# Optimization experiments

Hardware: AMD Instinct MI355X
Metric: run time of the kernel (lower is better)

## Reference

```python
import jax, jax.numpy as jnp
import numpy as np

B, SQ, SK, D, H = 2, 2048, 2048, 1024, 16
DK = D // H


def setup_inputs() -> dict:
    key = jax.random.key(0)
    ks = jax.random.split(key, 9)
    query = jax.random.normal(ks[0], (B, SQ, D), dtype=jnp.float32)
    k_in = jax.random.normal(ks[1], (B, SK, D), dtype=jnp.float32)
    v_in = jax.random.normal(ks[2], (B, SK, D), dtype=jnp.float32)
    # padding mask: 1 for valid tokens, 0 for padding; lengths in [SK//2, SK]
    lengths = jax.random.randint(ks[3], (B,), SK // 2, SK + 1)
    mask = (jnp.arange(SK)[None, :] < lengths[:, None]).astype(jnp.int32)
    scale = 1.0 / np.sqrt(D)
    Wq = jax.random.normal(ks[4], (D, D), dtype=jnp.float32) * scale
    Wk = jax.random.normal(ks[5], (D, D), dtype=jnp.float32) * scale
    Wv = jax.random.normal(ks[6], (D, D), dtype=jnp.float32) * scale
    Wo = jax.random.normal(ks[7], (D, D), dtype=jnp.float32) * scale
    return {"query": query, "key": k_in, "value": v_in, "mask": mask,
            "Wq": Wq, "Wk": Wk, "Wv": Wv, "Wo": Wo}


def reference(query, key, value, mask, Wq, Wk, Wv, Wo):
    # linear projections (torch Linear: x @ W.T)
    q = (query @ Wq.T).reshape(B, SQ, H, DK).transpose(0, 2, 1, 3)  # [B,H,SQ,DK]
    k = (key @ Wk.T).reshape(B, SK, H, DK).transpose(0, 2, 1, 3)    # [B,H,SK,DK]
    v = (value @ Wv.T).reshape(B, SK, H, DK).transpose(0, 2, 1, 3)  # [B,H,SK,DK]
    scores = jnp.einsum('bhqd,bhkd->bhqk', q, k) / jnp.sqrt(jnp.float32(DK))
    # padding mask: (B, SK) -> (B, 1, 1, SK)
    scores = jnp.where(mask[:, None, None, :] == 0, -jnp.inf, scores)
    # future (causal) mask
    future = jnp.triu(jnp.ones((SQ, SK), dtype=bool), k=1)
    scores = jnp.where(future[None, None], -jnp.inf, scores)
    attn = jax.nn.softmax(scores, axis=-1)
    attn = jnp.nan_to_num(attn, nan=0.0)
    ctx = jnp.einsum('bhqk,bhkd->bhqd', attn, v)
    ctx = ctx.transpose(0, 2, 1, 3).reshape(B, SQ, D)
    return ctx @ Wo.T
```

## Files before the change

### kernel.cpp

```cpp
#include <hip/hip_runtime.h>
#include <hip/hip_bf16.h>
#include <stdint.h>

#define BB 2
#define SS 2048
#define DD 1024
#define HH 16
#define DKK 64
#define MM (BB*SS)
#define LOG2E 1.4426950408889634f
#define QSCALE (0.125f * LOG2E)

typedef __attribute__((ext_vector_type(8))) short short8;
typedef __attribute__((ext_vector_type(8))) _Float16 half8;
typedef __attribute__((ext_vector_type(4))) float f32x4;

__device__ __forceinline__ short bfr(float f) {
    return (short)((__float_as_uint(f) + 0x8000u) >> 16);
}
__device__ __forceinline__ short f2h(float f) {
    _Float16 h = (_Float16)f;
    return __builtin_bit_cast(short, h);
}
__device__ __forceinline__ short8 cvt8(float4 a, float4 b) {
    short8 s;
    s[0] = bfr(a.x); s[1] = bfr(a.y); s[2] = bfr(a.z); s[3] = bfr(a.w);
    s[4] = bfr(b.x); s[5] = bfr(b.y); s[6] = bfr(b.z); s[7] = bfr(b.w);
    return s;
}

__device__ __forceinline__ void dma16(const void* g, void* l) {
    __builtin_amdgcn_global_load_lds(
        (const __attribute__((address_space(1))) uint32_t*)g,
        (__attribute__((address_space(3))) uint32_t*)(uintptr_t)l, 16, 0, 0);
}


__global__ __launch_bounds__(256) void cvt_all(const float* __restrict__ q,
                                               const float* __restrict__ k,
                                               const float* __restrict__ v,
                                               const float* __restrict__ wq,
                                               const float* __restrict__ wk,
                                               const float* __restrict__ wv,
                                               const float* __restrict__ wo,
                                               const int* __restrict__ mask,
                                               short* __restrict__ dst,
                                               float* __restrict__ Fb) {
    const size_t nth = (size_t)gridDim.x * blockDim.x;
    const size_t tid = (size_t)blockIdx.x * blockDim.x + threadIdx.x;
    if (tid < BB * SS) Fb[tid] = mask[tid] ? 0.f : -30000.f;
    for (size_t i8 = tid; i8 < (1u << 21); i8 += nth) {
        const size_t e = i8 * 8;
        const float* s;
        size_t rel;
        if (e < 4194304)        { s = q; rel = e; }
        else if (e < 8388608)   { s = k; rel = e - 4194304; }
        else if (e < 12582912)  { s = v; rel = e - 8388608; }
        else {
            const size_t we = e - 12582912;
            s = (we < 1048576) ? wq : (we < 2097152) ? wk : (we < 3145728) ? wv : wo;
            rel = we & 1048575;
        }
        const float4* p = (const float4*)(s + rel);
        *(short8*)(dst + e) = cvt8(p[0], p[1]);
    }
}

__global__ __launch_bounds__(256) void qkv_lds(const short* __restrict__ Abf,
                                               const short* __restrict__ Wbf,
                                               short* __restrict__ Qb,
                                               short* __restrict__ Kb,
                                               short* __restrict__ Vtb) {
    __shared__ __align__(16) short SH[128 * 132];
    short* As = SH;
    short* Ws = SH + 8192;
    const int z = blockIdx.z;
    const short* A = Abf + (size_t)z * 4194304;
    const short* W = Wbf + (size_t)z * 1048576;
    const int t = threadIdx.x, wave = t >> 6, lane = t & 63;
    const int la = lane & 15, quad = lane >> 4;
    const int wm = wave & 1, wn = wave >> 1;
    const int m0 = blockIdx.x * 128, n0 = blockIdx.y * 128;

    f32x4 acc[4][4];
    #pragma unroll
    for (int i = 0; i < 4; ++i)
        #pragma unroll
        for (int j = 0; j < 4; ++j) acc[i][j] = {0.f, 0.f, 0.f, 0.f};

    for (int k0 = 0; k0 < DD; k0 += 64) {
        #pragma unroll
        for (int j = 0; j < 4; ++j) {
            const int idx = j * 256 + t;
            const int row = idx >> 3, cpos = idx & 7;
            const int gc = cpos ^ (row & 7);
            dma16(A + (size_t)(m0 + row) * DD + k0 + gc * 8, As + idx * 8);
            dma16(W + (size_t)(n0 + row) * DD + k0 + gc * 8, Ws + idx * 8);
        }
        __syncthreads();
        #pragma unroll
        for (int kh = 0; kh < 2; ++kh) {
            short8 af[4], bf[4];
            #pragma unroll
            for (int mt = 0; mt < 4; ++mt) {
                const int row = wm * 64 + mt * 16 + la;
                af[mt] = *(const short8*)&As[row * 64 + (((kh << 2) | quad) ^ (row & 7)) * 8];
            }
            #pragma unroll
            for (int nt = 0; nt < 4; ++nt) {
                const int row = wn * 64 + nt * 16 + la;
                bf[nt] = *(const short8*)&Ws[row * 64 + (((kh << 2) | quad) ^ (row & 7)) * 8];
            }
            #pragma unroll
            for (int mt = 0; mt < 4; ++mt)
                #pragma unroll
                for (int nt = 0; nt < 4; ++nt)
                    acc[mt][nt] = __builtin_amdgcn_mfma_f32_16x16x32_bf16(af[mt], bf[nt], acc[mt][nt], 0, 0, 0);
        }
        __syncthreads();
    }

    #pragma unroll
    for (int mt = 0; mt < 4; ++mt)
        #pragma unroll
        for (int nt = 0; nt < 4; ++nt)
            #pragma unroll
            for (int r = 0; r < 4; ++r) {
                const float v = acc[mt][nt][r];
                const int mr = wm * 64 + mt * 16 + quad * 4 + r;
                const int nc = wn * 64 + nt * 16 + la;
                if (z == 2) SH[nc * 132 + mr] = f2h(v);
                else        SH[mr * 132 + nc] = bfr(z == 0 ? v * QSCALE : v);
            }
    __syncthreads();

    const int b = m0 >> 11;
    #pragma unroll
    for (int p = 0; p < 8; ++p) {
        const int idx = p * 256 + t;
        const int rr = idx >> 4, c8 = (idx & 15) * 8;
        short8 val = *(const short8*)&SH[rr * 132 + c8];
        if (z == 2) {
            const int n = n0 + rr, h2 = n >> 6, dk = n & 63;
            const int s = (m0 & 2047) + c8;
            *(short8*)(Vtb + ((size_t)(b * HH + h2) * DKK + dk) * SS + s) = val;
        } else {
            const int s = (m0 + rr) & 2047;
            const int n = n0 + c8, h2 = n >> 6, dk = n & 63;
            short* Y = (z == 0) ? Qb : Kb;
            *(short8*)(Y + ((size_t)(b * HH + h2) * SS + s) * DKK + dk) = val;
        }
    }
}

__global__ __launch_bounds__(256, 4) void attn4(const short* __restrict__ Q,
                                                const short* __restrict__ K,
                                                const short* __restrict__ Vt,
                                                const float* __restrict__ Fb,
                                                short* __restrict__ ctx) {
    const int b = blockIdx.z, h = blockIdx.y;
    const int qt = 15 - blockIdx.x;
    const int t = threadIdx.x, wave = t >> 6, lane = t & 63;
    const int la = lane & 15, quad = lane >> 4;

    __shared__ __align__(16) short Ks[64 * 72];
    __shared__ __align__(16) short Vs[64 * 72];
    __shared__ __align__(16) short Ps[128 * 76];

    const size_t kbase = ((size_t)(b * HH + h) * SS) * DKK;
    const size_t vbase = ((size_t)(b * HH + h) * DKK) * SS;

    short8 aq[2][2];
    #pragma unroll
    for (int mt = 0; mt < 2; ++mt)
        #pragma unroll
        for (int hf = 0; hf < 2; ++hf)
            aq[mt][hf] = *(const short8*)(Q + kbase
                + (size_t)(qt * 128 + wave * 32 + mt * 16 + la) * DKK + hf * 32 + quad * 8);

    const int srow = t >> 2, scol = (t & 3) * 16;
    short8 kr[2], vr[2];
    auto loadG = [&](int kt) {
        const short* kp = K + kbase + (size_t)(kt * 64 + srow) * DKK + scol;
        kr[0] = ((const short8*)kp)[0]; kr[1] = ((const short8*)kp)[1];
        const short* vp = Vt + vbase + (size_t)srow * SS + kt * 64 + scol;
        vr[0] = ((const short8*)vp)[0]; vr[1] = ((const short8*)vp)[1];
    };
    auto storeL = [&]() {
        *(short8*)&Ks[srow * 72 + scol]     = kr[0];
        *(short8*)&Ks[srow * 72 + scol + 8] = kr[1];
        *(short8*)&Vs[srow * 72 + scol]     = vr[0];
        *(short8*)&Vs[srow * 72 + scol + 8] = vr[1];
    };

    float rs[2][4] = {};
    f32x4 o[2][4];
    #pragma unroll
    for (int mt = 0; mt < 2; ++mt)
        #pragma unroll
        for (int dc = 0; dc < 4; ++dc) o[mt][dc] = {0.f, 0.f, 0.f, 0.f};

    const int lastkt = 2 * qt + 1;
    loadG(0); storeL(); __syncthreads();

    for (int kt = 0; kt <= lastkt; ++kt) {
        if (kt < lastkt) loadG(kt + 1);
        const bool diag   = (kt >= 2 * qt);
        const bool padded = (kt >= 16);

        #pragma unroll
        for (int ct = 0; ct < 4; ++ct) {
            short8 kb0 = *(const short8*)&Ks[(ct * 16 + la) * 72 + quad * 8];
            short8 kb1 = *(const short8*)&Ks[(ct * 16 + la) * 72 + 32 + quad * 8];
            f32x4 s[2];
            #pragma unroll
            for (int mt = 0; mt < 2; ++mt) {
                s[mt] = {0.f, 0.f, 0.f, 0.f};
                s[mt] = __builtin_amdgcn_mfma_f32_16x16x32_bf16(aq[mt][0], kb0, s[mt], 0, 0, 0);
                s[mt] = __builtin_amdgcn_mfma_f32_16x16x32_bf16(aq[mt][1], kb1, s[mt], 0, 0, 0);
            }
            const int col = kt * 64 + ct * 16 + la;
            const float bias = padded ? Fb[b * SS + col] : 0.f;
            #pragma unroll
            for (int mt = 0; mt < 2; ++mt) {
                const int row0 = qt * 128 + wave * 32 + mt * 16 + quad * 4;
                #pragma unroll
                for (int r = 0; r < 4; ++r) {
                    float x = s[mt][r] + bias;
                    if (diag && col > row0 + r) x = -30000.f;
                    const float p = exp2f(x);
                    rs[mt][r] += p;
                    Ps[(wave * 32 + mt * 16 + quad * 4 + r) * 76 + ct * 16 + la] = f2h(p);
                }
            }
        }

        #pragma unroll
        for (int c2 = 0; c2 < 2; ++c2) {
            half8 pa0 = *(const half8*)&Ps[(wave * 32 + la) * 76 + c2 * 32 + quad * 8];
            half8 pa1 = *(const half8*)&Ps[(wave * 32 + 16 + la) * 76 + c2 * 32 + quad * 8];
            #pragma unroll
            for (int dc = 0; dc < 4; ++dc) {
                half8 vb = *(const half8*)&Vs[(dc * 16 + la) * 72 + c2 * 32 + quad * 8];
                o[0][dc] = __builtin_amdgcn_mfma_f32_16x16x32_f16(pa0, vb, o[0][dc], 0, 0, 0);
                o[1][dc] = __builtin_amdgcn_mfma_f32_16x16x32_f16(pa1, vb, o[1][dc], 0, 0, 0);
            }
        }

        if (kt < lastkt) {
            __syncthreads();
            storeL();
            __syncthreads();
        }
    }

    #pragma unroll
    for (int mt = 0; mt < 2; ++mt) {
        #pragma unroll
        for (int r = 0; r < 4; ++r) {
            float v = rs[mt][r];
            v += __shfl_xor(v, 1, 64);
            v += __shfl_xor(v, 2, 64);
            v += __shfl_xor(v, 4, 64);
            v += __shfl_xor(v, 8, 64);
            const float inv = 1.0f / v;
            const int q = qt * 128 + wave * 32 + mt * 16 + quad * 4 + r;
            #pragma unroll
            for (int dc = 0; dc < 4; ++dc)
                ctx[((size_t)(b * SS + q) * DD) + h * DKK + dc * 16 + la] = bfr(o[mt][dc][r] * inv);
        }
    }
}

__global__ __launch_bounds__(256) void o_lds(const short* __restrict__ Ctx,
                                             const short* __restrict__ Wob,
                                             float* __restrict__ out) {
    __shared__ __align__(16) short As[128 * 64];
    __shared__ __align__(16) short Ws[64 * 64];
    const int t = threadIdx.x, wave = t >> 6, lane = t & 63;
    const int la = lane & 15, quad = lane >> 4;
    const int wm = wave & 1, wn = wave >> 1;
    const int m0 = blockIdx.x * 128, n0 = blockIdx.y * 64;

    f32x4 acc[4][2];
    #pragma unroll
    for (int i = 0; i < 4; ++i)
        #pragma unroll
        for (int j = 0; j < 2; ++j) acc[i][j] = {0.f, 0.f, 0.f, 0.f};

    for (int k0 = 0; k0 < DD; k0 += 64) {
        #pragma unroll
        for (int j = 0; j < 4; ++j) {
            const int idx = j * 256 + t;
            const int row = idx >> 3, cpos = idx & 7;
            const int gc = cpos ^ (row & 7);
            dma16(Ctx + (size_t)(m0 + row) * DD + k0 + gc * 8, (short*)As + idx * 8);
        }
        #pragma unroll
        for (int j = 0; j < 2; ++j) {
            const int idx = j * 256 + t;
            const int row = idx >> 3, cpos = idx & 7;
            const int gc = cpos ^ (row & 7);
            dma16(Wob + (size_t)(n0 + row) * DD + k0 + gc * 8, (short*)Ws + idx * 8);
        }
        __syncthreads();
        #pragma unroll
        for (int kh = 0; kh < 2; ++kh) {
            short8 af[4], bf[2];
            #pragma unroll
            for (int mt = 0; mt < 4; ++mt) {
                const int row = wm * 64 + mt * 16 + la;
                af[mt] = *(const short8*)&As[row * 64 + (((kh << 2) | quad) ^ (row & 7)) * 8];
            }
            #pragma unroll
            for (int nt = 0; nt < 2; ++nt) {
                const int row = wn * 32 + nt * 16 + la;
                bf[nt] = *(const short8*)&Ws[row * 64 + (((kh << 2) | quad) ^ (row & 7)) * 8];
            }
            #pragma unroll
            for (int mt = 0; mt < 4; ++mt)
                #pragma unroll
                for (int nt = 0; nt < 2; ++nt)
                    acc[mt][nt] = __builtin_amdgcn_mfma_f32_16x16x32_bf16(af[mt], bf[nt], acc[mt][nt], 0, 0, 0);
        }
        __syncthreads();
    }

    #pragma unroll
    for (int mt = 0; mt < 4; ++mt)
        #pragma unroll
        for (int nt = 0; nt < 2; ++nt)
            #pragma unroll
            for (int r = 0; r < 4; ++r) {
                const int m = m0 + wm * 64 + mt * 16 + quad * 4 + r;
                const int n = n0 + wn * 32 + nt * 16 + la;
                out[(size_t)m * DD + n] = acc[mt][nt][r];
            }
}

__global__ __launch_bounds__(256) void qkv_gemm(const float* __restrict__ Aq,
                                                const float* __restrict__ Ak,
                                                const float* __restrict__ Av,
                                                const float* __restrict__ Wq,
                                                const float* __restrict__ Wk,
                                                const float* __restrict__ Wv,
                                                short* __restrict__ Qb,
                                                short* __restrict__ Kb,
                                                short* __restrict__ Vtb) {
    __shared__ __align__(16) short As[2][128][40];
    __shared__ __align__(16) short Ws[2][128][40];
    const int z = blockIdx.z;
    const float* A = (z == 0) ? Aq : (z == 1) ? Ak : Av;
    const float* W = (z == 0) ? Wq : (z == 1) ? Wk : Wv;
    short* Y = (z == 0) ? Qb : (z == 1) ? Kb : Vtb;
    const int t = threadIdx.x, wave = t >> 6, lane = t & 63;
    const int la = lane & 15, quad = lane >> 4;
    const int wm = wave & 1, wn = wave >> 1;
    const int m0 = blockIdx.x * 128, n0 = blockIdx.y * 128;
    const int srow = t >> 1, scol = (t & 1) * 16;
    f32x4 acc[4][4];
    #pragma unroll
    for (int i = 0; i < 4; ++i)
        #pragma unroll
        for (int j = 0; j < 4; ++j) acc[i][j] = {0.f, 0.f, 0.f, 0.f};
    float4 ar[4], wr[4];
    auto loadG = [&](int i) {
        const int k0 = i * 32;
        const float4* pa = (const float4*)(A + (size_t)(m0 + srow) * DD + k0 + scol);
        ar[0] = pa[0]; ar[1] = pa[1]; ar[2] = pa[2]; ar[3] = pa[3];
        const float4* pw = (const float4*)(W + (size_t)(n0 + srow) * DD + k0 + scol);
        wr[0] = pw[0]; wr[1] = pw[1]; wr[2] = pw[2]; wr[3] = pw[3];
    };
    auto storeL = [&](int buf) {
        *(short8*)&As[buf][srow][scol]     = cvt8(ar[0], ar[1]);
        *(short8*)&As[buf][srow][scol + 8] = cvt8(ar[2], ar[3]);
        *(short8*)&Ws[buf][srow][scol]     = cvt8(wr[0], wr[1]);
        *(short8*)&Ws[buf][srow][scol + 8] = cvt8(wr[2], wr[3]);
    };
    loadG(0); storeL(0); __syncthreads();
    const int NIT = DD / 32;
    for (int i = 0; i < NIT; ++i) {
        if (i + 1 < NIT) loadG(i + 1);
        const int buf = i & 1;
        short8 af[4], bfv[4];
        #pragma unroll
        for (int mt = 0; mt < 4; ++mt)
            af[mt] = *(const short8*)&As[buf][wm * 64 + mt * 16 + la][quad * 8];
        #pragma unroll
        for (int nt = 0; nt < 4; ++nt)
            bfv[nt] = *(const short8*)&Ws[buf][wn * 64 + nt * 16 + la][quad * 8];
        #pragma unroll
        for (int mt = 0; mt < 4; ++mt)
            #pragma unroll
            for (int nt = 0; nt < 4; ++nt)
                acc[mt][nt] = __builtin_amdgcn_mfma_f32_16x16x32_bf16(af[mt], bfv[nt], acc[mt][nt], 0, 0, 0);
        if (i + 1 < NIT) { storeL((i + 1) & 1); __syncthreads(); }
    }
    #pragma unroll
    for (int mt = 0; mt < 4; ++mt)
        #pragma unroll
        for (int nt = 0; nt < 4; ++nt)
            #pragma unroll
            for (int r = 0; r < 4; ++r) {
                const int m = m0 + wm * 64 + mt * 16 + quad * 4 + r;
                const int n = n0 + wn * 64 + nt * 16 + la;
                const int b = m >> 11, s = m & (SS - 1);
                const int h = n >> 6, dk = n & 63;
                float v = acc[mt][nt][r];
                if (z == 0)      Y[(((size_t)(b * HH + h) * SS + s) * DKK) + dk] = bfr(v * QSCALE);
                else if (z == 1) Y[(((size_t)(b * HH + h) * SS + s) * DKK) + dk] = bfr(v);
                else             Y[(((size_t)(b * HH + h) * DKK + dk) * SS) + s] = bfr(v);
            }
}

__global__ __launch_bounds__(256) void attn_fused(const short* __restrict__ Q,
                                                  const short* __restrict__ K,
                                                  const short* __restrict__ Vt,
                                                  const int* __restrict__ mask,
                                                  short* __restrict__ ctx) {
    const int b = blockIdx.z, h = blockIdx.y, x = blockIdx.x;
    const int t = threadIdx.x, wave = t >> 6, lane = t & 63;
    const int la = lane & 15, quad = lane >> 4;
    __shared__ __align__(16) short Ks[2][64][72];
    __shared__ __align__(16) short Vs[2][64][72];
    __shared__ __align__(16) short Ps[64][72];
    const size_t kbase = ((size_t)(b * HH + h) * SS) * DKK;
    const size_t vbase = ((size_t)(b * HH + h) * DKK) * SS;
    const int srow = t >> 2, scol = (t & 3) * 16;
    short8 kr[2], vr[2];
    auto loadG = [&](int kt) {
        const short* kp = K + kbase + (size_t)(kt * 64 + srow) * DKK + scol;
        kr[0] = ((const short8*)kp)[0]; kr[1] = ((const short8*)kp)[1];
        const short* vp = Vt + vbase + (size_t)srow * SS + kt * 64 + scol;
        vr[0] = ((const short8*)vp)[0]; vr[1] = ((const short8*)vp)[1];
    };
    auto storeL = [&](int buf) {
        *(short8*)&Ks[buf][srow][scol]     = kr[0];
        *(short8*)&Ks[buf][srow][scol + 8] = kr[1];
        *(short8*)&Vs[buf][srow][scol]     = vr[0];
        *(short8*)&Vs[buf][srow][scol + 8] = vr[1];
    };
    #pragma unroll 1
    for (int phase = 0; phase < 2; ++phase) {
        const int qt = phase ? x : (31 - x);
        const size_t qbase = kbase + (size_t)(qt * 64) * DKK;
        const short8 aq0 = *(const short8*)(Q + qbase + (size_t)(wave * 16 + la) * DKK + quad * 8);
        const short8 aq1 = *(const short8*)(Q + qbase + (size_t)(wave * 16 + la) * DKK + 32 + quad * 8);
        float rs[4] = {0.f, 0.f, 0.f, 0.f};
        f32x4 o[4];
        #pragma unroll
        for (int dc = 0; dc < 4; ++dc) o[dc] = {0.f, 0.f, 0.f, 0.f};
        const int nkt = qt + 1;
        loadG(0); storeL(0); __syncthreads();
        for (int kt = 0; kt < nkt; ++kt) {
            if (kt + 1 < nkt) loadG(kt + 1);
            const int buf = kt & 1;
            const bool diag = (kt == qt);
            const bool padded = (kt >= 16);
            f32x4 s[4];
            #pragma unroll
            for (int ct = 0; ct < 4; ++ct) {
                s[ct] = {0.f, 0.f, 0.f, 0.f};
                short8 kb0 = *(const short8*)&Ks[buf][ct * 16 + la][quad * 8];
                short8 kb1 = *(const short8*)&Ks[buf][ct * 16 + la][32 + quad * 8];
                s[ct] = __builtin_amdgcn_mfma_f32_16x16x32_bf16(aq0, kb0, s[ct], 0, 0, 0);
                s[ct] = __builtin_amdgcn_mfma_f32_16x16x32_bf16(aq1, kb1, s[ct], 0, 0, 0);
            }
            const int rowq = qt * 64 + wave * 16 + quad * 4;
            #pragma unroll
            for (int ct = 0; ct < 4; ++ct) {
                const int col = kt * 64 + ct * 16 + la;
                const int mv = padded ? mask[b * SS + col] : 1;
                #pragma unroll
                for (int r = 0; r < 4; ++r) {
                    const bool dead = (diag && col > rowq + r) || (padded && mv == 0);
                    const float p = dead ? 0.f : exp2f(s[ct][r]);
                    rs[r] += p;
                    Ps[wave * 16 + quad * 4 + r][ct * 16 + la] = bfr(p);
                }
            }
            #pragma unroll
            for (int c2 = 0; c2 < 2; ++c2) {
                short8 pa = *(const short8*)&Ps[wave * 16 + la][c2 * 32 + quad * 8];
                #pragma unroll
                for (int dc = 0; dc < 4; ++dc) {
                    short8 vb = *(const short8*)&Vs[buf][dc * 16 + la][c2 * 32 + quad * 8];
                    o[dc] = __builtin_amdgcn_mfma_f32_16x16x32_bf16(pa, vb, o[dc], 0, 0, 0);
                }
            }
            if (kt + 1 < nkt) { storeL((kt + 1) & 1); __syncthreads(); }
        }
        #pragma unroll
        for (int r = 0; r < 4; ++r) {
            float v = rs[r];
            v += __shfl_xor(v, 1, 64);
            v += __shfl_xor(v, 2, 64);
            v += __shfl_xor(v, 4, 64);
            v += __shfl_xor(v, 8, 64);
            const float inv = 1.0f / v;
            const int q = qt * 64 + wave * 16 + quad * 4 + r;
            #pragma unroll
            for (int dc = 0; dc < 4; ++dc)
                ctx[((size_t)(b * SS + q) * DD) + h * DKK + dc * 16 + la] = bfr(o[dc][r] * inv);
        }
        __syncthreads();
    }
}

__global__ __launch_bounds__(256) void o_gemm(const short* __restrict__ Ctx,
                                              const float* __restrict__ Wo,
                                              float* __restrict__ out) {
    __shared__ __align__(16) short As[2][128][40];
    __shared__ __align__(16) short Ws[2][64][40];
    const int t = threadIdx.x, wave = t >> 6, lane = t & 63;
    const int la = lane & 15, quad = lane >> 4;
    const int wm = wave & 1, wn = wave >> 1;
    const int m0 = blockIdx.x * 128, n0 = blockIdx.y * 64;
    const int srowA = t >> 1, scolA = (t & 1) * 16;
    const int srowW = t >> 2, scolW = (t & 3) * 8;
    f32x4 acc[4][2];
    #pragma unroll
    for (int i = 0; i < 4; ++i)
        #pragma unroll
        for (int j = 0; j < 2; ++j) acc[i][j] = {0.f, 0.f, 0.f, 0.f};
    short8 ab[2];
    float4 wr[2];
    auto loadG = [&](int i) {
        const int k0 = i * 32;
        const short8* pa = (const short8*)(Ctx + (size_t)(m0 + srowA) * DD + k0 + scolA);
        ab[0] = pa[0]; ab[1] = pa[1];
        const float4* pw = (const float4*)(Wo + (size_t)(n0 + srowW) * DD + k0 + scolW);
        wr[0] = pw[0]; wr[1] = pw[1];
    };
    auto storeL = [&](int buf) {
        *(short8*)&As[buf][srowA][scolA]     = ab[0];
        *(short8*)&As[buf][srowA][scolA + 8] = ab[1];
        *(short8*)&Ws[buf][srowW][scolW]     = cvt8(wr[0], wr[1]);
    };
    loadG(0); storeL(0); __syncthreads();
    const int NIT = DD / 32;
    for (int i = 0; i < NIT; ++i) {
        if (i + 1 < NIT) loadG(i + 1);
        const int buf = i & 1;
        short8 af[4], bfv[2];
        #pragma unroll
        for (int mt = 0; mt < 4; ++mt)
            af[mt] = *(const short8*)&As[buf][wm * 64 + mt * 16 + la][quad * 8];
        #pragma unroll
        for (int nt = 0; nt < 2; ++nt)
            bfv[nt] = *(const short8*)&Ws[buf][wn * 32 + nt * 16 + la][quad * 8];
        #pragma unroll
        for (int mt = 0; mt < 4; ++mt)
            #pragma unroll
            for (int nt = 0; nt < 2; ++nt)
                acc[mt][nt] = __builtin_amdgcn_mfma_f32_16x16x32_bf16(af[mt], bfv[nt], acc[mt][nt], 0, 0, 0);
        if (i + 1 < NIT) { storeL((i + 1) & 1); __syncthreads(); }
    }
    #pragma unroll
    for (int mt = 0; mt < 4; ++mt)
        #pragma unroll
        for (int nt = 0; nt < 2; ++nt)
            #pragma unroll
            for (int r = 0; r < 4; ++r) {
                const int m = m0 + wm * 64 + mt * 16 + quad * 4 + r;
                const int n = n0 + wn * 32 + nt * 16 + la;
                out[(size_t)m * DD + n] = acc[mt][nt][r];
            }
}

extern "C" void kernel_launch(void* const* d_in, const int* in_sizes, int n_in,
                              void* d_out, int out_size, void* d_ws, size_t ws_size,
                              hipStream_t stream) {
    (void)in_sizes; (void)n_in; (void)out_size;
    const float* query = (const float*)d_in[0];
    const float* key   = (const float*)d_in[1];
    const float* value = (const float*)d_in[2];
    const int*   mask  = (const int*)  d_in[3];
    const float* Wq    = (const float*)d_in[4];
    const float* Wk    = (const float*)d_in[5];
    const float* Wv    = (const float*)d_in[6];
    const float* Wo    = (const float*)d_in[7];
    dim3 tb(256);

    if (ws_size >= (size_t)61000000) {
        short* Abf = (short*)d_ws;
        short* Wbf = Abf + 12582912;
        short* Qb  = Abf + 16777216;
        short* Kb  = Abf + 20971520;
        short* Vtb = Abf + 25165824;
        float* Fb  = (float*)(Abf + 29360128);
        short* Ctx = Abf;

        hipLaunchKernelGGL(cvt_all, dim3(1024), tb, 0, stream,
                           query, key, value, Wq, Wk, Wv, Wo, mask, Abf, Fb);
        hipLaunchKernelGGL(qkv_lds, dim3(32, 8, 3), tb, 0, stream, Abf, Wbf, Qb, Kb, Vtb);
        hipLaunchKernelGGL(attn4, dim3(16, 16, 2), tb, 0, stream,
                           (const short*)Qb, (const short*)Kb, (const short*)Vtb, Fb, Ctx);
        hipLaunchKernelGGL(o_lds, dim3(32, 16), tb, 0, stream,
                           (const short*)Ctx, (const short*)(Wbf + 3145728), (float*)d_out);
    } else {
        short* Qb  = (short*)d_ws;
        short* Kb  = Qb + (size_t)BB * HH * SS * DKK;
        short* Vtb = Kb + (size_t)BB * HH * SS * DKK;
        short* Ctx = Vtb + (size_t)BB * HH * SS * DKK;
        hipLaunchKernelGGL(qkv_gemm, dim3(MM / 128, DD / 128, 3), tb, 0, stream,
                           query, key, value, Wq, Wk, Wv, Qb, Kb, Vtb);
        hipLaunchKernelGGL(attn_fused, dim3(SS / 128, HH, BB), tb, 0, stream,
                           (const short*)Qb, (const short*)Kb, (const short*)Vtb, mask, Ctx);
        hipLaunchKernelGGL(o_gemm, dim3(MM / 128, DD / 64), tb, 0, stream,
                           (const short*)Ctx, Wo, (float*)d_out);
    }
}
```

Baseline: 286.2 us.

## Split attention KV loop across waves and shrink GEMM tiles for more blocks

The attention kernel now gives each block 64 query rows, with the four waves each handling every fourth key tile. K and V are read straight from global memory instead of being staged cooperatively in LDS. Partial outputs and row sums are reduced across waves through LDS at the end. The QKV and output projection GEMMs halve their M tile to 64, doubling the grid size to improve occupancy and CU fill. The trade-offs are repeated global K/V reads without LDS sharing, an extra cross-wave reduction pass, and lower per-block data reuse in the GEMMs.

```diff
diff --git a/kernel.cpp b/kernel.cpp
--- a/kernel.cpp
+++ b/kernel.cpp
@@ -71,39 +71,43 @@
                                                short* __restrict__ Qb,
                                                short* __restrict__ Kb,
                                                short* __restrict__ Vtb) {
-    __shared__ __align__(16) short SH[128 * 132];
+    __shared__ __align__(16) short SH[12288];
     short* As = SH;
-    short* Ws = SH + 8192;
+    short* Ws = SH + 4096;
     const int z = blockIdx.z;
     const short* A = Abf + (size_t)z * 4194304;
     const short* W = Wbf + (size_t)z * 1048576;
     const int t = threadIdx.x, wave = t >> 6, lane = t & 63;
     const int la = lane & 15, quad = lane >> 4;
     const int wm = wave & 1, wn = wave >> 1;
-    const int m0 = blockIdx.x * 128, n0 = blockIdx.y * 128;
-
-    f32x4 acc[4][4];
-    #pragma unroll
-    for (int i = 0; i < 4; ++i)
+    const int m0 = blockIdx.x * 64, n0 = blockIdx.y * 128;
+
+    f32x4 acc[2][4];
+    #pragma unroll
+    for (int i = 0; i < 2; ++i)
         #pragma unroll
         for (int j = 0; j < 4; ++j) acc[i][j] = {0.f, 0.f, 0.f, 0.f};
 
     for (int k0 = 0; k0 < DD; k0 += 64) {
+        #pragma unroll
+        for (int j = 0; j < 2; ++j) {
+            const int idx = j * 256 + t;
+            const int row = idx >> 3, gc = (idx & 7) ^ (row & 7);
+            dma16(A + (size_t)(m0 + row) * DD + k0 + gc * 8, As + idx * 8);
+        }
         #pragma unroll
         for (int j = 0; j < 4; ++j) {
             const int idx = j * 256 + t;
-            const int row = idx >> 3, cpos = idx & 7;
-            const int gc = cpos ^ (row & 7);
-            dma16(A + (size_t)(m0 + row) * DD + k0 + gc * 8, As + idx * 8);
+            const int row = idx >> 3, gc = (idx & 7) ^ (row & 7);
             dma16(W + (size_t)(n0 + row) * DD + k0 + gc * 8, Ws + idx * 8);
         }
         __syncthreads();
         #pragma unroll
         for (int kh = 0; kh < 2; ++kh) {
-            short8 af[4], bf[4];
-            #pragma unroll
-            for (int mt = 0; mt < 4; ++mt) {
-                const int row = wm * 64 + mt * 16 + la;
+            short8 af[2], bf[4];
+            #pragma unroll
+            for (int mt = 0; mt < 2; ++mt) {
+                const int row = wm * 32 + mt * 16 + la;
                 af[mt] = *(const short8*)&As[row * 64 + (((kh << 2) | quad) ^ (row & 7)) * 8];
             }
             #pragma unroll
@@ -112,7 +116,7 @@
                 bf[nt] = *(const short8*)&Ws[row * 64 + (((kh << 2) | quad) ^ (row & 7)) * 8];
             }
             #pragma unroll
-            for (int mt = 0; mt < 4; ++mt)
+            for (int mt = 0; mt < 2; ++mt)
                 #pragma unroll
                 for (int nt = 0; nt < 4; ++nt)
                     acc[mt][nt] = __builtin_amdgcn_mfma_f32_16x16x32_bf16(af[mt], bf[nt], acc[mt][nt], 0, 0, 0);
@@ -121,31 +125,33 @@
     }
 
     #pragma unroll
-    for (int mt = 0; mt < 4; ++mt)
+    for (int mt = 0; mt < 2; ++mt)
         #pragma unroll
         for (int nt = 0; nt < 4; ++nt)
             #pragma unroll
             for (int r = 0; r < 4; ++r) {
                 const float v = acc[mt][nt][r];
-                const int mr = wm * 64 + mt * 16 + quad * 4 + r;
+                const int mr = wm * 32 + mt * 16 + quad * 4 + r;
                 const int nc = wn * 64 + nt * 16 + la;
-                if (z == 2) SH[nc * 132 + mr] = f2h(v);
+                if (z == 2) SH[nc * 68 + mr] = f2h(v);
                 else        SH[mr * 132 + nc] = bfr(z == 0 ? v * QSCALE : v);
             }
     __syncthreads();
 
     const int b = m0 >> 11;
     #pragma unroll
-    for (int p = 0; p < 8; ++p) {
+    for (int p = 0; p < 4; ++p) {
         const int idx = p * 256 + t;
-        const int rr = idx >> 4, c8 = (idx & 15) * 8;
-        short8 val = *(const short8*)&SH[rr * 132 + c8];
         if (z == 2) {
+            const int rr = idx >> 3, c8 = (idx & 7) * 8;
+            short8 val = *(const short8*)&SH[rr * 68 + c8];
             const int n = n0 + rr, h2 = n >> 6, dk = n & 63;
-            const int s = (m0 & 2047) + c8;
+            const int s = (m0 & (SS - 1)) + c8;
             *(short8*)(Vtb + ((size_t)(b * HH + h2) * DKK + dk) * SS + s) = val;
         } else {
-            const int s = (m0 + rr) & 2047;
+            const int rr = idx >> 4, c8 = (idx & 15) * 8;
+            short8 val = *(const short8*)&SH[rr * 132 + c8];
+            const int s = (m0 + rr) & (SS - 1);
             const int n = n0 + c8, h2 = n >> 6, dk = n & 63;
             short* Y = (z == 0) ? Qb : Kb;
             *(short8*)(Y + ((size_t)(b * HH + h2) * SS + s) * DKK + dk) = val;
@@ -153,109 +159,94 @@
     }
 }
 
-__global__ __launch_bounds__(256, 4) void attn4(const short* __restrict__ Q,
-                                                const short* __restrict__ K,
-                                                const short* __restrict__ Vt,
-                                                const float* __restrict__ Fb,
-                                                short* __restrict__ ctx) {
+__global__ __launch_bounds__(256) void attn5(const short* __restrict__ Q,
+                                             const short* __restrict__ K,
+                                             const short* __restrict__ Vt,
+                                             const float* __restrict__ Fb,
+                                             short* __restrict__ ctx) {
     const int b = blockIdx.z, h = blockIdx.y;
-    const int qt = 15 - blockIdx.x;
+    const int qt = 31 - blockIdx.x;
     const int t = threadIdx.x, wave = t >> 6, lane = t & 63;
     const int la = lane & 15, quad = lane >> 4;
 
-    __shared__ __align__(16) short Ks[64 * 72];
-    __shared__ __align__(16) short Vs[64 * 72];
-    __shared__ __align__(16) short Ps[128 * 76];
+    __shared__ __align__(16) short Ps[4 * 4608];
+    __shared__ float Ls[4][16];
+    short* Pw = Ps + wave * 4608;
 
     const size_t kbase = ((size_t)(b * HH + h) * SS) * DKK;
     const size_t vbase = ((size_t)(b * HH + h) * DKK) * SS;
 
-    short8 aq[2][2];
-    #pragma unroll
-    for (int mt = 0; mt < 2; ++mt)
+    short8 aq[4][2];
+    #pragma unroll
+    for (int mt = 0; mt < 4; ++mt)
         #pragma unroll
         for (int hf = 0; hf < 2; ++hf)
             aq[mt][hf] = *(const short8*)(Q + kbase
-                + (size_t)(qt * 128 + wave * 32 + mt * 16 + la) * DKK + hf * 32 + quad * 8);
-
-    const int srow = t >> 2, scol = (t & 3) * 16;
-    short8 kr[2], vr[2];
-    auto loadG = [&](int kt) {
-        const short* kp = K + kbase + (size_t)(kt * 64 + srow) * DKK + scol;
-        kr[0] = ((const short8*)kp)[0]; kr[1] = ((const short8*)kp)[1];
-        const short* vp = Vt + vbase + (size_t)srow * SS + kt * 64 + scol;
-        vr[0] = ((const short8*)vp)[0]; vr[1] = ((const short8*)vp)[1];
-    };
-    auto storeL = [&]() {
-        *(short8*)&Ks[srow * 72 + scol]     = kr[0];
-        *(short8*)&Ks[srow * 72 + scol + 8] = kr[1];
-        *(short8*)&Vs[srow * 72 + scol]     = vr[0];
-        *(short8*)&Vs[srow * 72 + scol + 8] = vr[1];
-    };
-
-    float rs[2][4] = {};
-    f32x4 o[2][4];
-    #pragma unroll
-    for (int mt = 0; mt < 2; ++mt)
-        #pragma unroll
-        for (int dc = 0; dc < 4; ++dc) o[mt][dc] = {0.f, 0.f, 0.f, 0.f};
-
-    const int lastkt = 2 * qt + 1;
-    loadG(0); storeL(); __syncthreads();
-
-    for (int kt = 0; kt <= lastkt; ++kt) {
-        if (kt < lastkt) loadG(kt + 1);
-        const bool diag   = (kt >= 2 * qt);
+                + (size_t)(qt * 64 + mt * 16 + la) * DKK + hf * 32 + quad * 8);
+
+    f32x4 o[4][4];
+    float rs[4][4];
+    #pragma unroll
+    for (int mt = 0; mt < 4; ++mt)
+        #pragma unroll
+        for (int dc = 0; dc < 4; ++dc) {
+            o[mt][dc] = {0.f, 0.f, 0.f, 0.f};
+            rs[mt][dc] = 0.f;
+        }
+
+    for (int kt = wave; kt <= qt; kt += 4) {
+        const bool diag   = (kt == qt);
         const bool padded = (kt >= 16);
 
         #pragma unroll
         for (int ct = 0; ct < 4; ++ct) {
-            short8 kb0 = *(const short8*)&Ks[(ct * 16 + la) * 72 + quad * 8];
-            short8 kb1 = *(const short8*)&Ks[(ct * 16 + la) * 72 + 32 + quad * 8];
-            f32x4 s[2];
-            #pragma unroll
-            for (int mt = 0; mt < 2; ++mt) {
+            const short* kp = K + kbase + (size_t)(kt * 64 + ct * 16 + la) * DKK;
+            short8 kb0 = *(const short8*)(kp + quad * 8);
+            short8 kb1 = *(const short8*)(kp + 32 + quad * 8);
+            const int col = kt * 64 + ct * 16 + la;
+            const float bias = padded ? Fb[b * SS + col] : 0.f;
+            f32x4 s[4];
+            #pragma unroll
+            for (int mt = 0; mt < 4; ++mt) {
                 s[mt] = {0.f, 0.f, 0.f, 0.f};
                 s[mt] = __builtin_amdgcn_mfma_f32_16x16x32_bf16(aq[mt][0], kb0, s[mt], 0, 0, 0);
                 s[mt] = __builtin_amdgcn_mfma_f32_16x16x32_bf16(aq[mt][1], kb1, s[mt], 0, 0, 0);
             }
-            const int col = kt * 64 + ct * 16 + la;
-            const float bias = padded ? Fb[b * SS + col] : 0.f;
-            #pragma unroll
-            for (int mt = 0; mt < 2; ++mt) {
-                const int row0 = qt * 128 + wave * 32 + mt * 16 + quad * 4;
+            #pragma unroll
+            for (int mt = 0; mt < 4; ++mt) {
+                const int row0 = qt * 64 + mt * 16 + quad * 4;
                 #pragma unroll
                 for (int r = 0; r < 4; ++r) {
                     float x = s[mt][r] + bias;
                     if (diag && col > row0 + r) x = -30000.f;
                     const float p = exp2f(x);
                     rs[mt][r] += p;
-                    Ps[(wave * 32 + mt * 16 + quad * 4 + r) * 76 + ct * 16 + la] = f2h(p);
+                    Pw[(mt * 16 + quad * 4 + r) * 72 + ct * 16 + la] = f2h(p);
                 }
             }
         }
 
         #pragma unroll
         for (int c2 = 0; c2 < 2; ++c2) {
-            half8 pa0 = *(const half8*)&Ps[(wave * 32 + la) * 76 + c2 * 32 + quad * 8];
-            half8 pa1 = *(const half8*)&Ps[(wave * 32 + 16 + la) * 76 + c2 * 32 + quad * 8];
+            half8 pa[4];
+            #pragma unroll
+            for (int mt = 0; mt < 4; ++mt)
+                pa[mt] = *(const half8*)&Pw[(mt * 16 + la) * 72 + c2 * 32 + quad * 8];
             #pragma unroll
             for (int dc = 0; dc < 4; ++dc) {
-                half8 vb = *(const half8*)&Vs[(dc * 16 + la) * 72 + c2 * 32 + quad * 8];
-                o[0][dc] = __builtin_amdgcn_mfma_f32_16x16x32_f16(pa0, vb, o[0][dc], 0, 0, 0);
-                o[1][dc] = __builtin_amdgcn_mfma_f32_16x16x32_f16(pa1, vb, o[1][dc], 0, 0, 0);
-            }
-        }
-
-        if (kt < lastkt) {
-            __syncthreads();
-            storeL();
-            __syncthreads();
-        }
-    }
-
-    #pragma unroll
-    for (int mt = 0; mt < 2; ++mt) {
+                half8 vb = *(const half8*)(Vt + vbase + (size_t)(dc * 16 + la) * SS
+                                           + kt * 64 + c2 * 32 + quad * 8);
+                #pragma unroll
+                for (int mt = 0; mt < 4; ++mt)
+                    o[mt][dc] = __builtin_amdgcn_mfma_f32_16x16x32_f16(pa[mt], vb, o[mt][dc], 0, 0, 0);
+            }
+        }
+    }
+
+    __syncthreads();
+    float* Fs = (float*)Ps;
+    #pragma unroll 1
+    for (int mt = 0; mt < 4; ++mt) {
         #pragma unroll
         for (int r = 0; r < 4; ++r) {
             float v = rs[mt][r];
@@ -263,53 +254,57 @@
             v += __shfl_xor(v, 2, 64);
             v += __shfl_xor(v, 4, 64);
             v += __shfl_xor(v, 8, 64);
-            const float inv = 1.0f / v;
-            const int q = qt * 128 + wave * 32 + mt * 16 + quad * 4 + r;
+            if (la == 0) Ls[wave][quad * 4 + r] = v;
             #pragma unroll
             for (int dc = 0; dc < 4; ++dc)
-                ctx[((size_t)(b * SS + q) * DD) + h * DKK + dc * 16 + la] = bfr(o[mt][dc][r] * inv);
-        }
+                Fs[wave * 1024 + (quad * 4 + r) * 64 + dc * 16 + la] = o[mt][dc][r];
+        }
+        __syncthreads();
+        #pragma unroll
+        for (int i = 0; i < 4; ++i) {
+            const int idx = i * 256 + t;
+            const int row = idx >> 6, colx = idx & 63;
+            const float osum = Fs[row * 64 + colx] + Fs[1024 + row * 64 + colx]
+                             + Fs[2048 + row * 64 + colx] + Fs[3072 + row * 64 + colx];
+            const float l = Ls[0][row] + Ls[1][row] + Ls[2][row] + Ls[3][row];
+            const int q = qt * 64 + mt * 16 + row;
+            ctx[((size_t)(b * SS + q) * DD) + h * DKK + colx] = bfr(osum / l);
+        }
+        __syncthreads();
     }
 }
 
 __global__ __launch_bounds__(256) void o_lds(const short* __restrict__ Ctx,
                                              const short* __restrict__ Wob,
                                              float* __restrict__ out) {
-    __shared__ __align__(16) short As[128 * 64];
+    __shared__ __align__(16) short As[64 * 64];
     __shared__ __align__(16) short Ws[64 * 64];
     const int t = threadIdx.x, wave = t >> 6, lane = t & 63;
     const int la = lane & 15, quad = lane >> 4;
     const int wm = wave & 1, wn = wave >> 1;
-    const int m0 = blockIdx.x * 128, n0 = blockIdx.y * 64;
-
-    f32x4 acc[4][2];
-    #pragma unroll
-    for (int i = 0; i < 4; ++i)
+    const int m0 = blockIdx.x * 64, n0 = blockIdx.y * 64;
+
+    f32x4 acc[2][2];
+    #pragma unroll
+    for (int i = 0; i < 2; ++i)
         #pragma unroll
         for (int j = 0; j < 2; ++j) acc[i][j] = {0.f, 0.f, 0.f, 0.f};
 
     for (int k0 = 0; k0 < DD; k0 += 64) {
-        #pragma unroll
-        for (int j = 0; j < 4; ++j) {
-            const int idx = j * 256 + t;
-            const int row = idx >> 3, cpos = idx & 7;
-            const int gc = cpos ^ (row & 7);
-            dma16(Ctx + (size_t)(m0 + row) * DD + k0 + gc * 8, (short*)As + idx * 8);
-        }
         #pragma unroll
         for (int j = 0; j < 2; ++j) {
             const int idx = j * 256 + t;
-            const int row = idx >> 3, cpos = idx & 7;
-            const int gc = cpos ^ (row & 7);
+            const int row = idx >> 3, gc = (idx & 7) ^ (row & 7);
+            dma16(Ctx + (size_t)(m0 + row) * DD + k0 + gc * 8, (short*)As + idx * 8);
             dma16(Wob + (size_t)(n0 + row) * DD + k0 + gc * 8, (short*)Ws + idx * 8);
         }
         __syncthreads();
         #pragma unroll
         for (int kh = 0; kh < 2; ++kh) {
-            short8 af[4], bf[2];
-            #pragma unroll
-            for (int mt = 0; mt < 4; ++mt) {
-                const int row = wm * 64 + mt * 16 + la;
+            short8 af[2], bf[2];
+            #pragma unroll
+            for (int mt = 0; mt < 2; ++mt) {
+                const int row = wm * 32 + mt * 16 + la;
                 af[mt] = *(const short8*)&As[row * 64 + (((kh << 2) | quad) ^ (row & 7)) * 8];
             }
             #pragma unroll
@@ -318,7 +313,7 @@
                 bf[nt] = *(const short8*)&Ws[row * 64 + (((kh << 2) | quad) ^ (row & 7)) * 8];
             }
             #pragma unroll
-            for (int mt = 0; mt < 4; ++mt)
+            for (int mt = 0; mt < 2; ++mt)
                 #pragma unroll
                 for (int nt = 0; nt < 2; ++nt)
                     acc[mt][nt] = __builtin_amdgcn_mfma_f32_16x16x32_bf16(af[mt], bf[nt], acc[mt][nt], 0, 0, 0);
@@ -327,12 +322,12 @@
     }
 
     #pragma unroll
-    for (int mt = 0; mt < 4; ++mt)
+    for (int mt = 0; mt < 2; ++mt)
         #pragma unroll
         for (int nt = 0; nt < 2; ++nt)
             #pragma unroll
             for (int r = 0; r < 4; ++r) {
-                const int m = m0 + wm * 64 + mt * 16 + quad * 4 + r;
+                const int m = m0 + wm * 32 + mt * 16 + quad * 4 + r;
                 const int n = n0 + wn * 32 + nt * 16 + la;
                 out[(size_t)m * DD + n] = acc[mt][nt][r];
             }
@@ -593,10 +588,10 @@
 
         hipLaunchKernelGGL(cvt_all, dim3(1024), tb, 0, stream,
                            query, key, value, Wq, Wk, Wv, Wo, mask, Abf, Fb);
-        hipLaunchKernelGGL(qkv_lds, dim3(32, 8, 3), tb, 0, stream, Abf, Wbf, Qb, Kb, Vtb);
-        hipLaunchKernelGGL(attn4, dim3(16, 16, 2), tb, 0, stream,
+        hipLaunchKernelGGL(qkv_lds, dim3(64, 8, 3), tb, 0, stream, Abf, Wbf, Qb, Kb, Vtb);
+        hipLaunchKernelGGL(attn5, dim3(32, 16, 2), tb, 0, stream,
                            (const short*)Qb, (const short*)Kb, (const short*)Vtb, Fb, Ctx);
-        hipLaunchKernelGGL(o_lds, dim3(32, 16), tb, 0, stream,
+        hipLaunchKernelGGL(o_lds, dim3(64, 16), tb, 0, stream,
                            (const short*)Ctx, (const short*)(Wbf + 3145728), (float*)d_out);
     } else {
         short* Qb  = (short*)d_ws;
```

Result: slower. 296.4 us (+3.6%).
